# Kernel optimization log

Hardware: AMD Instinct MI355X
Metric: run time of the kernel (lower is better)

## Reference

```python
import jax, jax.numpy as jnp
import numpy as np

N_NODES = 50000
N_EDGES = 800000
D = 256
N_LAYERS = 3
BN_EPS = 1e-5


def setup_inputs() -> dict:
    key = jax.random.key(0)
    ks = jax.random.split(key, 7)
    x = jax.random.normal(ks[0], (N_NODES, D), dtype=jnp.float32)
    Wl = jax.random.normal(ks[1], (N_LAYERS, D, D), dtype=jnp.float32)
    bl = jax.random.normal(ks[2], (N_LAYERS, D), dtype=jnp.float32)
    Wr = jax.random.normal(ks[3], (N_LAYERS, D, D), dtype=jnp.float32)
    gamma = jax.random.uniform(ks[4], (N_LAYERS, D), dtype=jnp.float32)
    beta = jax.random.normal(ks[5], (N_LAYERS, D), dtype=jnp.float32)
    edge_index = jax.random.randint(ks[6], (2, N_EDGES), 0, N_NODES, dtype=jnp.int64)
    return {"x": x, "Wl": Wl, "bl": bl, "Wr": Wr, "gamma": gamma,
            "beta": beta, "edge_index": edge_index}


def reference(x, Wl, bl, Wr, gamma, beta, edge_index):
    """3-layer GNN: SAGEConv(mean) -> BatchNorm1d(train) -> ReLU per layer."""
    src = edge_index[0]
    dst = edge_index[1]
    n = x.shape[0]
    # In-degree (mean-aggregation denominator); clamp to avoid div-by-zero.
    deg = jax.ops.segment_sum(jnp.ones((src.shape[0],), dtype=x.dtype), dst,
                              num_segments=n)
    deg = jnp.maximum(deg, 1.0)[:, None]  # [N, 1]
    n_layers = Wl.shape[0]
    for i in range(n_layers):
        # --- SAGEConv: mean-aggregate neighbor messages, then linear ---
        agg = jax.ops.segment_sum(x[src], dst, num_segments=n) / deg  # [N, D]
        h = agg @ Wl[i] + bl[i] + x @ Wr[i]                           # [N, D]
        # --- BatchNorm1d (training mode: batch stats, biased variance) ---
        mu = jnp.mean(h, axis=0)
        var = jnp.mean(jnp.square(h - mu), axis=0)
        h = (h - mu) * jax.lax.rsqrt(var + BN_EPS) * gamma[i] + beta[i]
        # --- ReLU ---
        x = jax.nn.relu(h)
    return x
```

## Files before the change

kernel.cpp:

```cpp
#include <hip/hip_runtime.h>

#define N_NODES 50000
#define N_PAD   50176
#define N_EDGES 800000
#define DIM     256
#define KDIM    512
#define BN_EPS  1e-5f
#define SCAN_NB ((N_NODES + 1023) / 1024)

typedef __attribute__((ext_vector_type(8))) short short8;
typedef __attribute__((ext_vector_type(4))) float floatx4;

__device__ __forceinline__ float bf2f(unsigned short u) {
    return __uint_as_float(((unsigned int)u) << 16);
}
__device__ __forceinline__ unsigned short f2bf(float f) {
    unsigned int b = __float_as_uint(f);
    b = (b + 0x7FFF + ((b >> 16) & 1)) >> 16;
    return (unsigned short)b;
}

__device__ __forceinline__ void gload_lds16(const void* g, void* l) {
    __builtin_amdgcn_global_load_lds(
        (const __attribute__((address_space(1))) unsigned int*)g,
        (__attribute__((address_space(3))) unsigned int*)l, 16, 0, 0);
}


__global__ void k_deg_count(const int* __restrict__ dst, int* __restrict__ degi) {
    int e = blockIdx.x * blockDim.x + threadIdx.x;
    if (e < N_EDGES) atomicAdd(&degi[dst[e]], 1);
}

__global__ void k_scan1(const int* __restrict__ degi, int* __restrict__ off,
                        float* __restrict__ inv_deg, int* __restrict__ bsums) {
    __shared__ int buf[1024];
    int i = blockIdx.x * 1024 + threadIdx.x;
    int v = (i < N_NODES) ? degi[i] : 0;
    if (i < N_NODES) inv_deg[i] = 1.0f / (float)max(v, 1);
    buf[threadIdx.x] = v;
    __syncthreads();
    for (int s = 1; s < 1024; s <<= 1) {
        int t = (threadIdx.x >= s) ? buf[threadIdx.x - s] : 0;
        __syncthreads();
        buf[threadIdx.x] += t;
        __syncthreads();
    }
    if (i < N_NODES) off[i + 1] = buf[threadIdx.x];
    if (threadIdx.x == 1023) bsums[blockIdx.x] = buf[1023];
    if (i == 0) off[0] = 0;
}

__global__ void k_scan2(int* __restrict__ bsums) {
    int t = threadIdx.x;
    int orig = (t < SCAN_NB) ? bsums[t] : 0;
    int v = orig;
    for (int s = 1; s < 64; s <<= 1) {
        int u = __shfl_up(v, s, 64);
        if (t >= s) v += u;
    }
    if (t < SCAN_NB) bsums[t] = v - orig;
}

__global__ void k_scan3(int* __restrict__ off, const int* __restrict__ bsums) {
    int i = blockIdx.x * 1024 + threadIdx.x;
    if (i < N_NODES) off[i + 1] += bsums[blockIdx.x];
}

__global__ void k_fill(const int* __restrict__ src, const int* __restrict__ dst,
                       const int* __restrict__ off, int* __restrict__ cursor,
                       int* __restrict__ csr_src) {
    int e = blockIdx.x * blockDim.x + threadIdx.x;
    if (e < N_EDGES) {
        int d = dst[e];
        int pos = atomicAdd(&cursor[d], 1);
        csr_src[off[d] + pos] = src[e];
    }
}


__global__ void k_prep_w(const float* __restrict__ Wl, const float* __restrict__ Wr,
                         unsigned short* __restrict__ Wcat) {
    int gid = blockIdx.x * blockDim.x + threadIdx.x;
    if (gid >= 3 * DIM * KDIM) return;
    int k = gid & (KDIM - 1);
    int n = (gid >> 9) & (DIM - 1);
    int l = gid >> 17;
    float v = (k < DIM) ? Wl[(size_t)l * DIM * DIM + (size_t)k * DIM + n]
                        : Wr[(size_t)l * DIM * DIM + (size_t)(k - DIM) * DIM + n];
    Wcat[gid] = f2bf(v);
}


__global__ void k_x2bf(const float* __restrict__ x, unsigned short* __restrict__ Acat) {
    size_t i = (size_t)blockIdx.x * blockDim.x + threadIdx.x;
    if (i >= (size_t)N_NODES * (DIM / 4)) return;
    int node = (int)(i >> 6);
    int c = ((int)i & 63) * 4;
    float4 v = ((const float4*)x)[i];
    ushort4 o; o.x = f2bf(v.x); o.y = f2bf(v.y); o.z = f2bf(v.z); o.w = f2bf(v.w);
    *(ushort4*)&Acat[(size_t)node * KDIM + DIM + c] = o;
}


__device__ __forceinline__ void addv(float* a, uint4 v) {
    unsigned int w[4] = {v.x, v.y, v.z, v.w};
    #pragma unroll
    for (int q = 0; q < 4; ++q) {
        a[2 * q + 0] += bf2f((unsigned short)(w[q] & 0xFFFF));
        a[2 * q + 1] += bf2f((unsigned short)(w[q] >> 16));
    }
}

__global__ __launch_bounds__(256) void k_aggregate(
        const unsigned short* __restrict__ Acat_x,
        const int* __restrict__ off,
        const int* __restrict__ csr_src,
        const float* __restrict__ inv_deg,
        unsigned short* __restrict__ Acat_agg) {
    int gid = blockIdx.x * blockDim.x + threadIdx.x;
    int node = gid >> 5;
    int lane = threadIdx.x & 31;
    if (node >= N_NODES) return;
    int beg = off[node], end = off[node + 1];
    float a[8];
    #pragma unroll
    for (int q = 0; q < 8; ++q) a[q] = 0.f;
    const unsigned short* xb = Acat_x + DIM + lane * 8;

    int e = beg;
    for (; e + 4 <= end; e += 4) {
        int s0 = csr_src[e + 0];
        int s1 = csr_src[e + 1];
        int s2 = csr_src[e + 2];
        int s3 = csr_src[e + 3];
        uint4 v0 = *(const uint4*)(xb + (size_t)s0 * KDIM);
        uint4 v1 = *(const uint4*)(xb + (size_t)s1 * KDIM);
        uint4 v2 = *(const uint4*)(xb + (size_t)s2 * KDIM);
        uint4 v3 = *(const uint4*)(xb + (size_t)s3 * KDIM);
        addv(a, v0); addv(a, v1); addv(a, v2); addv(a, v3);
    }
    for (; e < end; ++e) {
        uint4 v = *(const uint4*)(xb + (size_t)csr_src[e] * KDIM);
        addv(a, v);
    }

    float inv = inv_deg[node];
    unsigned int w[4];
    #pragma unroll
    for (int q = 0; q < 4; ++q)
        w[q] = (unsigned int)f2bf(a[2 * q] * inv) |
               ((unsigned int)f2bf(a[2 * q + 1] * inv) << 16);
    uint4 o; o.x = w[0]; o.y = w[1]; o.z = w[2]; o.w = w[3];
    *(uint4*)&Acat_agg[(size_t)node * KDIM + lane * 8] = o;
}


__global__ __launch_bounds__(256) void k_gemm_mfma(
        const unsigned short* __restrict__ A,
        const unsigned short* __restrict__ Bt,
        const float* __restrict__ bias, unsigned short* __restrict__ H,
        float* __restrict__ ssum, float* __restrict__ ssq) {
    __shared__ __align__(16) short Alds[128 * 32];
    __shared__ __align__(16) short Blds[128 * 32];
    int tid = threadIdx.x;
    int wid = tid >> 6;
    int lane = tid & 63;
    int wm = wid >> 1, wn = wid & 1;
    int brow = blockIdx.x * 128;
    int bcol = blockIdx.y * 128;

    floatx4 acc[4][4];
    #pragma unroll
    for (int i = 0; i < 4; ++i)
        #pragma unroll
        for (int j = 0; j < 4; ++j) acc[i][j] = (floatx4){0.f, 0.f, 0.f, 0.f};

    int st_r0 = (lane >> 2);
    int st_s  = lane & 3;
    int rb = lane & 15;
    int k16r = lane >> 4;

    for (int kt = 0; kt < KDIM / 32; ++kt) {
        int k0 = kt * 32;
        #pragma unroll
        for (int q = 0; q < 2; ++q) {
            int c = wid * 2 + q;
            int r = c * 16 + st_r0;
            int k16 = (st_s - (r >> 1)) & 3;
            gload_lds16(A + (size_t)(brow + r) * KDIM + k0 + k16 * 8, &Alds[c * 512]);
            gload_lds16(Bt + (size_t)(bcol + r) * KDIM + k0 + k16 * 8, &Blds[c * 512]);
        }
        __syncthreads();

        short8 af[4], bfr[4];
        #pragma unroll
        for (int i = 0; i < 4; ++i) {
            int ra = wm * 64 + i * 16 + rb;
            int sa = (k16r + (ra >> 1)) & 3;
            af[i] = *(const short8*)&Alds[ra * 32 + sa * 8];
            int rc = wn * 64 + i * 16 + rb;
            int sc = (k16r + (rc >> 1)) & 3;
            bfr[i] = *(const short8*)&Blds[rc * 32 + sc * 8];
        }
        #pragma unroll
        for (int i = 0; i < 4; ++i)
            #pragma unroll
            for (int j = 0; j < 4; ++j)
                acc[i][j] = __builtin_amdgcn_mfma_f32_16x16x32_bf16(
                    af[i], bfr[j], acc[i][j], 0, 0, 0);
        __syncthreads();
    }

    int rg = lane >> 4;
    #pragma unroll
    for (int j = 0; j < 4; ++j) {
        int col = bcol + wn * 64 + j * 16 + rb;
        float bv = bias[col];
        float s = 0.f, s2 = 0.f;
        #pragma unroll
        for (int i = 0; i < 4; ++i) {
            #pragma unroll
            for (int q = 0; q < 4; ++q) {
                int row = brow + wm * 64 + i * 16 + rg * 4 + q;
                float o = acc[i][j][q] + bv;
                unsigned short hb = f2bf(o);
                if (row < N_NODES) {
                    H[(size_t)row * DIM + col] = hb;
                    float of = bf2f(hb);
                    s += of;
                    s2 = fmaf(of, of, s2);
                }
            }
        }
        s  += __shfl_xor(s, 16);
        s  += __shfl_xor(s, 32);
        s2 += __shfl_xor(s2, 16);
        s2 += __shfl_xor(s2, 32);
        if (rg == 0) {
            atomicAdd(&ssum[col], s);
            atomicAdd(&ssq[col], s2);
        }
    }
}


__global__ void k_norm_relu(const unsigned short* __restrict__ H,
                            const float* __restrict__ ssum,
                            const float* __restrict__ ssq,
                            const float* __restrict__ gamma,
                            const float* __restrict__ beta,
                            float* __restrict__ outF,
                            unsigned short* __restrict__ Acat, int last) {
    __shared__ float sc[DIM], sh[DIM];
    {
        int c = threadIdx.x;
        float mu  = ssum[c] * (1.0f / N_NODES);
        float var = ssq[c] * (1.0f / N_NODES) - mu * mu;
        float rstd = rsqrtf(var + BN_EPS);
        float s = rstd * gamma[c];
        sc[c] = s;
        sh[c] = beta[c] - mu * s;
    }
    __syncthreads();
    size_t total8 = (size_t)N_NODES * DIM / 8;
    for (size_t i = (size_t)blockIdx.x * blockDim.x + threadIdx.x; i < total8;
         i += (size_t)gridDim.x * blockDim.x) {
        uint4 raw = ((const uint4*)H)[i];
        int node = (int)(i >> 5);
        int c = ((int)i & 31) * 8;
        unsigned int w[4] = {raw.x, raw.y, raw.z, raw.w};
        float o[8];
        #pragma unroll
        for (int q = 0; q < 4; ++q) {
            float lo = bf2f((unsigned short)(w[q] & 0xFFFF));
            float hi = bf2f((unsigned short)(w[q] >> 16));
            o[q * 2 + 0] = fmaxf(fmaf(lo, sc[c + q * 2 + 0], sh[c + q * 2 + 0]), 0.f);
            o[q * 2 + 1] = fmaxf(fmaf(hi, sc[c + q * 2 + 1], sh[c + q * 2 + 1]), 0.f);
        }
        if (last) {
            float4 f0 = make_float4(o[0], o[1], o[2], o[3]);
            float4 f1 = make_float4(o[4], o[5], o[6], o[7]);
            *(float4*)(outF + (size_t)node * DIM + c)     = f0;
            *(float4*)(outF + (size_t)node * DIM + c + 4) = f1;
        } else {
            uint4 u;
            unsigned int uw[4];
            #pragma unroll
            for (int q = 0; q < 4; ++q)
                uw[q] = (unsigned int)f2bf(o[q * 2 + 0]) |
                        ((unsigned int)f2bf(o[q * 2 + 1]) << 16);
            u.x = uw[0]; u.y = uw[1]; u.z = uw[2]; u.w = uw[3];
            *(uint4*)&Acat[(size_t)node * KDIM + DIM + c] = u;
        }
    }
}


extern "C" void kernel_launch(void* const* d_in, const int* in_sizes, int n_in,
                              void* d_out, int out_size, void* d_ws, size_t ws_size,
                              hipStream_t stream) {
    const float* x0    = (const float*)d_in[0];
    const float* Wl    = (const float*)d_in[1];
    const float* bl    = (const float*)d_in[2];
    const float* Wr    = (const float*)d_in[3];
    const float* gamma = (const float*)d_in[4];
    const float* beta  = (const float*)d_in[5];
    const int*   ei    = (const int*)d_in[6];
    const int* e_src = ei;
    const int* e_dst = ei + N_EDGES;

    char* ws = (char*)d_ws;
    size_t off = 0;
    auto alloc = [&](size_t bytes) { char* p = ws + off; off = (off + bytes + 255) & ~(size_t)255; return p; };
    unsigned short* Acat = (unsigned short*)alloc((size_t)N_PAD * KDIM * 2);
    unsigned short* Hbuf = (unsigned short*)alloc((size_t)N_PAD * DIM * 2);
    unsigned short* Wcat = (unsigned short*)alloc((size_t)3 * DIM * KDIM * 2);
    int*   csr_src = (int*)alloc((size_t)N_EDGES * 4);
    int*   csr_off = (int*)alloc((size_t)(N_NODES + 1) * 4);
    int*   degi    = (int*)alloc((size_t)N_NODES * 4);
    int*   cursor  = (int*)alloc((size_t)N_NODES * 4);
    int*   bsums   = (int*)alloc((size_t)SCAN_NB * 4);
    float* inv_deg = (float*)alloc((size_t)N_NODES * 4);
    float* stats   = (float*)alloc((size_t)3 * 2 * DIM * 4);
    (void)ws_size;

    hipMemsetAsync(degi, 0, (size_t)N_NODES * 4, stream);
    hipMemsetAsync(cursor, 0, (size_t)N_NODES * 4, stream);
    hipMemsetAsync(stats, 0, (size_t)3 * 2 * DIM * 4, stream);

    int eb = (N_EDGES + 255) / 256;
    k_deg_count<<<eb, 256, 0, stream>>>(e_dst, degi);
    k_scan1<<<SCAN_NB, 1024, 0, stream>>>(degi, csr_off, inv_deg, bsums);
    k_scan2<<<1, 64, 0, stream>>>(bsums);
    k_scan3<<<SCAN_NB, 1024, 0, stream>>>(csr_off, bsums);
    k_fill<<<eb, 256, 0, stream>>>(e_src, e_dst, csr_off, cursor, csr_src);
    k_prep_w<<<(3 * DIM * KDIM + 255) / 256, 256, 0, stream>>>(Wl, Wr, Wcat);
    k_x2bf<<<(N_NODES * (DIM / 4) + 255) / 256, 256, 0, stream>>>(x0, Acat);

    for (int l = 0; l < 3; ++l) {
        float* ssum_l = stats + (size_t)l * 2 * DIM;
        float* ssq_l  = ssum_l + DIM;
        k_aggregate<<<(N_NODES * 32 + 255) / 256, 256, 0, stream>>>(
            Acat, csr_off, csr_src, inv_deg, Acat);
        k_gemm_mfma<<<dim3((N_NODES + 127) / 128, DIM / 128), 256, 0, stream>>>(
            Acat, Wcat + (size_t)l * DIM * KDIM, bl + (size_t)l * DIM, Hbuf, ssum_l, ssq_l);
        k_norm_relu<<<2048, 256, 0, stream>>>(Hbuf, ssum_l, ssq_l,
                                              gamma + (size_t)l * DIM, beta + (size_t)l * DIM,
                                              (float*)d_out, Acat, (l == 2) ? 1 : 0);
    }
}
```

Baseline: 578.1 us.

## Double-buffer GEMM LDS tiles and unroll aggregation gather by eight

The GEMM kernel now keeps two LDS buffers and issues the global-to-LDS loads for the next K tile before computing on the current one, so global memory latency can overlap the MFMA work, with one sync per iteration instead of two. The neighbour aggregation loop gains an 8-way unrolled stage so more independent row gathers are in flight per thread. The cost is double the GEMM shared memory and more registers in the aggregation kernel, which may reduce occupancy. The double-buffer relies on the single barrier at the end of each iteration to order the async LDS writes against reads of the other buffer.

```diff
diff --git a/kernel.cpp b/kernel.cpp
--- a/kernel.cpp
+++ b/kernel.cpp
@@ -129,15 +129,23 @@
     const unsigned short* xb = Acat_x + DIM + lane * 8;
 
     int e = beg;
+    for (; e + 8 <= end; e += 8) {
+        uint4 v0 = *(const uint4*)(xb + (size_t)csr_src[e + 0] * KDIM);
+        uint4 v1 = *(const uint4*)(xb + (size_t)csr_src[e + 1] * KDIM);
+        uint4 v2 = *(const uint4*)(xb + (size_t)csr_src[e + 2] * KDIM);
+        uint4 v3 = *(const uint4*)(xb + (size_t)csr_src[e + 3] * KDIM);
+        uint4 v4 = *(const uint4*)(xb + (size_t)csr_src[e + 4] * KDIM);
+        uint4 v5 = *(const uint4*)(xb + (size_t)csr_src[e + 5] * KDIM);
+        uint4 v6 = *(const uint4*)(xb + (size_t)csr_src[e + 6] * KDIM);
+        uint4 v7 = *(const uint4*)(xb + (size_t)csr_src[e + 7] * KDIM);
+        addv(a, v0); addv(a, v1); addv(a, v2); addv(a, v3);
+        addv(a, v4); addv(a, v5); addv(a, v6); addv(a, v7);
+    }
     for (; e + 4 <= end; e += 4) {
-        int s0 = csr_src[e + 0];
-        int s1 = csr_src[e + 1];
-        int s2 = csr_src[e + 2];
-        int s3 = csr_src[e + 3];
-        uint4 v0 = *(const uint4*)(xb + (size_t)s0 * KDIM);
-        uint4 v1 = *(const uint4*)(xb + (size_t)s1 * KDIM);
-        uint4 v2 = *(const uint4*)(xb + (size_t)s2 * KDIM);
-        uint4 v3 = *(const uint4*)(xb + (size_t)s3 * KDIM);
+        uint4 v0 = *(const uint4*)(xb + (size_t)csr_src[e + 0] * KDIM);
+        uint4 v1 = *(const uint4*)(xb + (size_t)csr_src[e + 1] * KDIM);
+        uint4 v2 = *(const uint4*)(xb + (size_t)csr_src[e + 2] * KDIM);
+        uint4 v3 = *(const uint4*)(xb + (size_t)csr_src[e + 3] * KDIM);
         addv(a, v0); addv(a, v1); addv(a, v2); addv(a, v3);
     }
     for (; e < end; ++e) {
@@ -161,8 +169,8 @@
         const unsigned short* __restrict__ Bt,
         const float* __restrict__ bias, unsigned short* __restrict__ H,
         float* __restrict__ ssum, float* __restrict__ ssq) {
-    __shared__ __align__(16) short Alds[128 * 32];
-    __shared__ __align__(16) short Blds[128 * 32];
+    __shared__ __align__(16) short Alds[2][128 * 32];
+    __shared__ __align__(16) short Blds[2][128 * 32];
     int tid = threadIdx.x;
     int wid = tid >> 6;
     int lane = tid & 63;
@@ -181,27 +189,33 @@
     int rb = lane & 15;
     int k16r = lane >> 4;
 
-    for (int kt = 0; kt < KDIM / 32; ++kt) {
+    auto stage = [&](int buf, int kt) {
         int k0 = kt * 32;
         #pragma unroll
         for (int q = 0; q < 2; ++q) {
             int c = wid * 2 + q;
             int r = c * 16 + st_r0;
             int k16 = (st_s - (r >> 1)) & 3;
-            gload_lds16(A + (size_t)(brow + r) * KDIM + k0 + k16 * 8, &Alds[c * 512]);
-            gload_lds16(Bt + (size_t)(bcol + r) * KDIM + k0 + k16 * 8, &Blds[c * 512]);
-        }
-        __syncthreads();
+            gload_lds16(A + (size_t)(brow + r) * KDIM + k0 + k16 * 8, &Alds[buf][c * 512]);
+            gload_lds16(Bt + (size_t)(bcol + r) * KDIM + k0 + k16 * 8, &Blds[buf][c * 512]);
+        }
+    };
+
+    stage(0, 0);
+    __syncthreads();
+    int cur = 0;
+    for (int kt = 0; kt < KDIM / 32; ++kt) {
+        if (kt + 1 < KDIM / 32) stage(cur ^ 1, kt + 1);
 
         short8 af[4], bfr[4];
         #pragma unroll
         for (int i = 0; i < 4; ++i) {
             int ra = wm * 64 + i * 16 + rb;
             int sa = (k16r + (ra >> 1)) & 3;
-            af[i] = *(const short8*)&Alds[ra * 32 + sa * 8];
+            af[i] = *(const short8*)&Alds[cur][ra * 32 + sa * 8];
             int rc = wn * 64 + i * 16 + rb;
             int sc = (k16r + (rc >> 1)) & 3;
-            bfr[i] = *(const short8*)&Blds[rc * 32 + sc * 8];
+            bfr[i] = *(const short8*)&Blds[cur][rc * 32 + sc * 8];
         }
         #pragma unroll
         for (int i = 0; i < 4; ++i)
@@ -210,6 +224,7 @@
                 acc[i][j] = __builtin_amdgcn_mfma_f32_16x16x32_bf16(
                     af[i], bfr[j], acc[i][j], 0, 0, 0);
         __syncthreads();
+        cur ^= 1;
     }
 
     int rg = lane >> 4;
```

Result: no change. 584.9 us (+1.2%).

## Fuse BatchNorm+ReLU into next layer's gather and widen GEMM K-tile

Applied to the files above, without the earlier changes.

For layers after the first, the aggregation kernel now reads the raw pre-norm H buffer and applies BatchNorm scale/shift and ReLU on the fly to every gathered neighbour row. It also writes the normalized self row into the concatenated A matrix, which removes the separate norm/ReLU pass for intermediate layers. The gather loop is unrolled to 8 edges, and the GEMM moves to a 64-wide K tile with XOR-swizzled LDS, halving the number of barrier-separated iterations. The cost is redundant normalize math per gathered edge, plus more LDS per block.

```diff
diff --git a/kernel.cpp b/kernel.cpp
--- a/kernel.cpp
+++ b/kernel.cpp
@@ -7,6 +7,7 @@
 #define KDIM    512
 #define BN_EPS  1e-5f
 #define SCAN_NB ((N_NODES + 1023) / 1024)
+#define NT      (KDIM / 64)
 
 typedef __attribute__((ext_vector_type(8))) short short8;
 typedef __attribute__((ext_vector_type(4))) float floatx4;
@@ -103,46 +104,103 @@
 }
 
 
-__device__ __forceinline__ void addv(float* a, uint4 v) {
+template<int NORM>
+__device__ __forceinline__ void accum8(float* a, uint4 v,
+                                       const float* sc, const float* sh) {
     unsigned int w[4] = {v.x, v.y, v.z, v.w};
     #pragma unroll
     for (int q = 0; q < 4; ++q) {
-        a[2 * q + 0] += bf2f((unsigned short)(w[q] & 0xFFFF));
-        a[2 * q + 1] += bf2f((unsigned short)(w[q] >> 16));
+        float lo = bf2f((unsigned short)(w[q] & 0xFFFF));
+        float hi = bf2f((unsigned short)(w[q] >> 16));
+        if (NORM) {
+            lo = fmaxf(fmaf(lo, sc[2 * q], sh[2 * q]), 0.f);
+            hi = fmaxf(fmaf(hi, sc[2 * q + 1], sh[2 * q + 1]), 0.f);
+        }
+        a[2 * q + 0] += lo;
+        a[2 * q + 1] += hi;
+    }
+}
+
+template<int NORM>
+__device__ __forceinline__ void gather_loop(float* a, const unsigned short* xb,
+                                            int sstride, const int* csr_src,
+                                            int beg, int end,
+                                            const float* sc, const float* sh) {
+    int e = beg;
+    for (; e + 8 <= end; e += 8) {
+        uint4 v0 = *(const uint4*)(xb + (size_t)csr_src[e + 0] * sstride);
+        uint4 v1 = *(const uint4*)(xb + (size_t)csr_src[e + 1] * sstride);
+        uint4 v2 = *(const uint4*)(xb + (size_t)csr_src[e + 2] * sstride);
+        uint4 v3 = *(const uint4*)(xb + (size_t)csr_src[e + 3] * sstride);
+        uint4 v4 = *(const uint4*)(xb + (size_t)csr_src[e + 4] * sstride);
+        uint4 v5 = *(const uint4*)(xb + (size_t)csr_src[e + 5] * sstride);
+        uint4 v6 = *(const uint4*)(xb + (size_t)csr_src[e + 6] * sstride);
+        uint4 v7 = *(const uint4*)(xb + (size_t)csr_src[e + 7] * sstride);
+        accum8<NORM>(a, v0, sc, sh); accum8<NORM>(a, v1, sc, sh);
+        accum8<NORM>(a, v2, sc, sh); accum8<NORM>(a, v3, sc, sh);
+        accum8<NORM>(a, v4, sc, sh); accum8<NORM>(a, v5, sc, sh);
+        accum8<NORM>(a, v6, sc, sh); accum8<NORM>(a, v7, sc, sh);
+    }
+    for (; e + 4 <= end; e += 4) {
+        uint4 v0 = *(const uint4*)(xb + (size_t)csr_src[e + 0] * sstride);
+        uint4 v1 = *(const uint4*)(xb + (size_t)csr_src[e + 1] * sstride);
+        uint4 v2 = *(const uint4*)(xb + (size_t)csr_src[e + 2] * sstride);
+        uint4 v3 = *(const uint4*)(xb + (size_t)csr_src[e + 3] * sstride);
+        accum8<NORM>(a, v0, sc, sh); accum8<NORM>(a, v1, sc, sh);
+        accum8<NORM>(a, v2, sc, sh); accum8<NORM>(a, v3, sc, sh);
+    }
+    for (; e < end; ++e) {
+        uint4 v = *(const uint4*)(xb + (size_t)csr_src[e] * sstride);
+        accum8<NORM>(a, v, sc, sh);
     }
 }
 
 __global__ __launch_bounds__(256) void k_aggregate(
-        const unsigned short* __restrict__ Acat_x,
-        const int* __restrict__ off,
-        const int* __restrict__ csr_src,
+        const unsigned short* __restrict__ src, int sstride,
+        const int* __restrict__ off, const int* __restrict__ csr_src,
         const float* __restrict__ inv_deg,
-        unsigned short* __restrict__ Acat_agg) {
+        unsigned short* __restrict__ Acat,
+        const float* __restrict__ ssum, const float* __restrict__ ssq,
+        const float* __restrict__ gamma, const float* __restrict__ beta,
+        int norm_mode) {
     int gid = blockIdx.x * blockDim.x + threadIdx.x;
     int node = gid >> 5;
     int lane = threadIdx.x & 31;
     if (node >= N_NODES) return;
+    int c0 = lane * 8;
     int beg = off[node], end = off[node + 1];
     float a[8];
     #pragma unroll
     for (int q = 0; q < 8; ++q) a[q] = 0.f;
-    const unsigned short* xb = Acat_x + DIM + lane * 8;
-
-    int e = beg;
-    for (; e + 4 <= end; e += 4) {
-        int s0 = csr_src[e + 0];
-        int s1 = csr_src[e + 1];
-        int s2 = csr_src[e + 2];
-        int s3 = csr_src[e + 3];
-        uint4 v0 = *(const uint4*)(xb + (size_t)s0 * KDIM);
-        uint4 v1 = *(const uint4*)(xb + (size_t)s1 * KDIM);
-        uint4 v2 = *(const uint4*)(xb + (size_t)s2 * KDIM);
-        uint4 v3 = *(const uint4*)(xb + (size_t)s3 * KDIM);
-        addv(a, v0); addv(a, v1); addv(a, v2); addv(a, v3);
-    }
-    for (; e < end; ++e) {
-        uint4 v = *(const uint4*)(xb + (size_t)csr_src[e] * KDIM);
-        addv(a, v);
+    float sc[8], sh[8];
+    const unsigned short* xb = src + c0;
+
+    if (norm_mode) {
+        #pragma unroll
+        for (int q = 0; q < 8; ++q) {
+            int c = c0 + q;
+            float mu  = ssum[c] * (1.0f / N_NODES);
+            float var = ssq[c] * (1.0f / N_NODES) - mu * mu;
+            float rs  = rsqrtf(var + BN_EPS);
+            sc[q] = rs * gamma[c];
+            sh[q] = beta[c] - mu * sc[q];
+        }
+        uint4 ov = *(const uint4*)(xb + (size_t)node * sstride);
+        unsigned int w[4] = {ov.x, ov.y, ov.z, ov.w};
+        unsigned int uw[4];
+        #pragma unroll
+        for (int q = 0; q < 4; ++q) {
+            float lo = fmaxf(fmaf(bf2f((unsigned short)(w[q] & 0xFFFF)),
+                                  sc[2 * q], sh[2 * q]), 0.f);
+            float hi = fmaxf(fmaf(bf2f((unsigned short)(w[q] >> 16)),
+                                  sc[2 * q + 1], sh[2 * q + 1]), 0.f);
+            uw[q] = (unsigned int)f2bf(lo) | ((unsigned int)f2bf(hi) << 16);
+        }
+        uint4 ox; ox.x = uw[0]; ox.y = uw[1]; ox.z = uw[2]; ox.w = uw[3];
+        *(uint4*)&Acat[(size_t)node * KDIM + DIM + c0] = ox;
+        gather_loop<1>(a, xb, sstride, csr_src, beg, end, sc, sh);
+    } else {
+        gather_loop<0>(a, xb, sstride, csr_src, beg, end, sc, sh);
     }
 
     float inv = inv_deg[node];
@@ -152,7 +210,7 @@
         w[q] = (unsigned int)f2bf(a[2 * q] * inv) |
                ((unsigned int)f2bf(a[2 * q + 1] * inv) << 16);
     uint4 o; o.x = w[0]; o.y = w[1]; o.z = w[2]; o.w = w[3];
-    *(uint4*)&Acat_agg[(size_t)node * KDIM + lane * 8] = o;
+    *(uint4*)&Acat[(size_t)node * KDIM + c0] = o;
 }
 
 
@@ -161,8 +219,8 @@
         const unsigned short* __restrict__ Bt,
         const float* __restrict__ bias, unsigned short* __restrict__ H,
         float* __restrict__ ssum, float* __restrict__ ssq) {
-    __shared__ __align__(16) short Alds[128 * 32];
-    __shared__ __align__(16) short Blds[128 * 32];
+    __shared__ __align__(16) short Alds[128 * 64];
+    __shared__ __align__(16) short Blds[128 * 64];
     int tid = threadIdx.x;
     int wid = tid >> 6;
     int lane = tid & 63;
@@ -176,39 +234,43 @@
         #pragma unroll
         for (int j = 0; j < 4; ++j) acc[i][j] = (floatx4){0.f, 0.f, 0.f, 0.f};
 
-    int st_r0 = (lane >> 2);
-    int st_s  = lane & 3;
+    int st_row = lane >> 3;
+    int st_s   = lane & 7;
+    int sg_st  = st_s ^ st_row;
     int rb = lane & 15;
     int k16r = lane >> 4;
 
-    for (int kt = 0; kt < KDIM / 32; ++kt) {
-        int k0 = kt * 32;
-        #pragma unroll
-        for (int q = 0; q < 2; ++q) {
-            int c = wid * 2 + q;
-            int r = c * 16 + st_r0;
-            int k16 = (st_s - (r >> 1)) & 3;
-            gload_lds16(A + (size_t)(brow + r) * KDIM + k0 + k16 * 8, &Alds[c * 512]);
-            gload_lds16(Bt + (size_t)(bcol + r) * KDIM + k0 + k16 * 8, &Blds[c * 512]);
+    for (int kt = 0; kt < NT; ++kt) {
+        int k0 = kt * 64;
+        #pragma unroll
+        for (int q = 0; q < 4; ++q) {
+            int c = wid * 4 + q;
+            int r = c * 8 + st_row;
+            gload_lds16(A + (size_t)(brow + r) * KDIM + k0 + sg_st * 8,
+                        &Alds[c * 512]);
+            gload_lds16(Bt + (size_t)(bcol + r) * KDIM + k0 + sg_st * 8,
+                        &Blds[c * 512]);
         }
         __syncthreads();
 
-        short8 af[4], bfr[4];
-        #pragma unroll
-        for (int i = 0; i < 4; ++i) {
-            int ra = wm * 64 + i * 16 + rb;
-            int sa = (k16r + (ra >> 1)) & 3;
-            af[i] = *(const short8*)&Alds[ra * 32 + sa * 8];
-            int rc = wn * 64 + i * 16 + rb;
-            int sc = (k16r + (rc >> 1)) & 3;
-            bfr[i] = *(const short8*)&Blds[rc * 32 + sc * 8];
-        }
-        #pragma unroll
-        for (int i = 0; i < 4; ++i)
+        #pragma unroll
+        for (int kk = 0; kk < 2; ++kk) {
+            short8 af[4], bfr[4];
             #pragma unroll
-            for (int j = 0; j < 4; ++j)
-                acc[i][j] = __builtin_amdgcn_mfma_f32_16x16x32_bf16(
-                    af[i], bfr[j], acc[i][j], 0, 0, 0);
+            for (int i = 0; i < 4; ++i) {
+                int ra = wm * 64 + i * 16 + rb;
+                int s_st = (kk * 4 + k16r) ^ (rb & 7);
+                af[i] = *(const short8*)&Alds[ra * 64 + s_st * 8];
+                int rc = wn * 64 + i * 16 + rb;
+                bfr[i] = *(const short8*)&Blds[rc * 64 + s_st * 8];
+            }
+            #pragma unroll
+            for (int i = 0; i < 4; ++i)
+                #pragma unroll
+                for (int j = 0; j < 4; ++j)
+                    acc[i][j] = __builtin_amdgcn_mfma_f32_16x16x32_bf16(
+                        af[i], bfr[j], acc[i][j], 0, 0, 0);
+        }
         __syncthreads();
     }
 
@@ -245,13 +307,10 @@
 }
 
 
-__global__ void k_norm_relu(const unsigned short* __restrict__ H,
-                            const float* __restrict__ ssum,
-                            const float* __restrict__ ssq,
-                            const float* __restrict__ gamma,
-                            const float* __restrict__ beta,
-                            float* __restrict__ outF,
-                            unsigned short* __restrict__ Acat, int last) {
+__global__ void k_out(const unsigned short* __restrict__ H,
+                      const float* __restrict__ ssum, const float* __restrict__ ssq,
+                      const float* __restrict__ gamma, const float* __restrict__ beta,
+                      float* __restrict__ outF) {
     __shared__ float sc[DIM], sh[DIM];
     {
         int c = threadIdx.x;
@@ -278,21 +337,10 @@
             o[q * 2 + 0] = fmaxf(fmaf(lo, sc[c + q * 2 + 0], sh[c + q * 2 + 0]), 0.f);
             o[q * 2 + 1] = fmaxf(fmaf(hi, sc[c + q * 2 + 1], sh[c + q * 2 + 1]), 0.f);
         }
-        if (last) {
-            float4 f0 = make_float4(o[0], o[1], o[2], o[3]);
-            float4 f1 = make_float4(o[4], o[5], o[6], o[7]);
-            *(float4*)(outF + (size_t)node * DIM + c)     = f0;
-            *(float4*)(outF + (size_t)node * DIM + c + 4) = f1;
-        } else {
-            uint4 u;
-            unsigned int uw[4];
-            #pragma unroll
-            for (int q = 0; q < 4; ++q)
-                uw[q] = (unsigned int)f2bf(o[q * 2 + 0]) |
-                        ((unsigned int)f2bf(o[q * 2 + 1]) << 16);
-            u.x = uw[0]; u.y = uw[1]; u.z = uw[2]; u.w = uw[3];
-            *(uint4*)&Acat[(size_t)node * KDIM + DIM + c] = u;
-        }
+        float4 f0 = make_float4(o[0], o[1], o[2], o[3]);
+        float4 f1 = make_float4(o[4], o[5], o[6], o[7]);
+        *(float4*)(outF + (size_t)node * DIM + c)     = f0;
+        *(float4*)(outF + (size_t)node * DIM + c + 4) = f1;
     }
 }
 
@@ -338,15 +386,26 @@
     k_prep_w<<<(3 * DIM * KDIM + 255) / 256, 256, 0, stream>>>(Wl, Wr, Wcat);
     k_x2bf<<<(N_NODES * (DIM / 4) + 255) / 256, 256, 0, stream>>>(x0, Acat);
 
+    int ab = (N_NODES * 32 + 255) / 256;
     for (int l = 0; l < 3; ++l) {
         float* ssum_l = stats + (size_t)l * 2 * DIM;
         float* ssq_l  = ssum_l + DIM;
-        k_aggregate<<<(N_NODES * 32 + 255) / 256, 256, 0, stream>>>(
-            Acat, csr_off, csr_src, inv_deg, Acat);
-        k_gemm_mfma<<<dim3((N_NODES + 127) / 128, DIM / 128), 256, 0, stream>>>(
-            Acat, Wcat + (size_t)l * DIM * KDIM, bl + (size_t)l * DIM, Hbuf, ssum_l, ssq_l);
-        k_norm_relu<<<2048, 256, 0, stream>>>(Hbuf, ssum_l, ssq_l,
-                                              gamma + (size_t)l * DIM, beta + (size_t)l * DIM,
-                                              (float*)d_out, Acat, (l == 2) ? 1 : 0);
-    }
-}
+        if (l == 0) {
+            k_aggregate<<<ab, 256, 0, stream>>>(
+                Acat + DIM, KDIM, csr_off, csr_src, inv_deg, Acat,
+                stats, stats, gamma, beta, 0);
+        } else {
+            float* ssum_p = stats + (size_t)(l - 1) * 2 * DIM;
+            k_aggregate<<<ab, 256, 0, stream>>>(
+                Hbuf, DIM, csr_off, csr_src, inv_deg, Acat,
+                ssum_p, ssum_p + DIM, gamma + (size_t)(l - 1) * DIM,
+                beta + (size_t)(l - 1) * DIM, 1);
+        }
+        k_gemm_mfma<<<dim3(N_PAD / 128, DIM / 128), 256, 0, stream>>>(
+            Acat, Wcat + (size_t)l * DIM * KDIM, bl + (size_t)l * DIM, Hbuf,
+            ssum_l, ssq_l);
+    }
+    float* ssum2 = stats + (size_t)2 * 2 * DIM;
+    k_out<<<2048, 256, 0, stream>>>(Hbuf, ssum2, ssum2 + DIM,
+                                    gamma + 2 * DIM, beta + 2 * DIM, (float*)d_out);
+}
```

Result: slower. 593.9 us (+2.7%).
